# Optimization experiments

Hardware: AMD Instinct MI355X
Metric: run time of the kernel (lower is better)

## Reference

```python
import jax, jax.numpy as jnp
import numpy as np

START_INDEX = 1


def _lstm_cell(x, h, c, W_ih, W_hh, b_ih, b_hh):
    # PyTorch LSTM cell: gate order i, f, g, o
    gates = x @ W_ih.T + b_ih + h @ W_hh.T + b_hh  # [B, 4H]
    i, f, g, o = jnp.split(gates, 4, axis=-1)
    c_new = jax.nn.sigmoid(f) * c + jax.nn.sigmoid(i) * jnp.tanh(g)
    h_new = jax.nn.sigmoid(o) * jnp.tanh(c_new)
    return h_new, c_new


def setup_inputs() -> dict:
    key = jax.random.key(0)
    ks = jax.random.split(key, 13)
    B, C, E, H, V = 32, 512, 512, 512, 32000
    s = 0.05  # keep gates in non-saturated range

    def w(k, shape):
        return jax.random.normal(k, shape, dtype=jnp.float32) * s

    return {
        "context": jax.random.normal(ks[0], (B, C), dtype=jnp.float32),
        "emb": w(ks[1], (V, E)),
        "W_ih_l0": w(ks[2], (4 * H, E + C)),
        "W_hh_l0": w(ks[3], (4 * H, H)),
        "b_ih_l0": w(ks[4], (4 * H,)),
        "b_hh_l0": w(ks[5], (4 * H,)),
        "W_ih_l1": w(ks[6], (4 * H, H)),
        "W_hh_l1": w(ks[7], (4 * H, H)),
        "b_ih_l1": w(ks[8], (4 * H,)),
        "b_hh_l1": w(ks[9], (4 * H,)),
        "W_out": w(ks[10], (V, H)),
        "b_out": w(ks[11], (V,)),
        "max_len": 64,
    }


def reference(context, emb, W_ih_l0, W_hh_l0, b_ih_l0, b_hh_l0,
              W_ih_l1, W_hh_l1, b_ih_l1, b_hh_l1, W_out, b_out, max_len):
    B = context.shape[0]
    H = W_hh_l0.shape[1]
    tok0 = jnp.full((B,), START_INDEX, dtype=jnp.int32)
    z = jnp.zeros((B, H), dtype=context.dtype)

    def step(carry, _):
        tok, h0, c0, h1, c1 = carry
        ex = emb[tok]                                   # [B, E] embedding lookup
        inp = jnp.concatenate([ex, context], axis=-1)   # [B, E+C]
        h0, c0 = _lstm_cell(inp, h0, c0, W_ih_l0, W_hh_l0, b_ih_l0, b_hh_l0)
        h1, c1 = _lstm_cell(h0, h1, c1, W_ih_l1, W_hh_l1, b_ih_l1, b_hh_l1)
        logits = h1 @ W_out.T + b_out                   # [B, V]
        logp = jax.nn.log_softmax(logits, axis=-1)
        tok_next = jnp.argmax(logp, axis=-1).astype(jnp.int32)  # greedy feedback (detached)
        return (tok_next, h0, c0, h1, c1), logp

    _, out = jax.lax.scan(step, (tok0, z, z, z, z), None, length=max_len)
    return jnp.transpose(out, (1, 0, 2))                # [B, max_len, V]
```

## Files before the change

### kernel.cpp

```cpp
#include <hip/hip_runtime.h>
#include <math.h>

#define BB 32
#define HH 512
#define VV 32000
#define TT 64

#define OFF_H0T  0
#define OFF_H1T  32768
#define OFF_C0   65536
#define OFF_C1   81920
#define OFF_PC0  98304
#define OFF_AMAX 163840

__device__ __forceinline__ float sigmoidf_(float x) { return 1.0f / (1.0f + expf(-x)); }

__device__ __forceinline__ float dot4(const float4 wv, const float4 xv) {
    return wv.x * xv.x + wv.y * xv.y + wv.z * xv.z + wv.w * xv.w;
}
__device__ __forceinline__ void bcast_fma(float* A, const float4 wv,
                                          const float4 x0, const float4 x1,
                                          const float4 x2, const float4 x3) {
    A[0] += wv.x * x0.x + wv.y * x1.x + wv.z * x2.x + wv.w * x3.x;
    A[1] += wv.x * x0.y + wv.y * x1.y + wv.z * x2.y + wv.w * x3.y;
    A[2] += wv.x * x0.z + wv.y * x1.z + wv.z * x2.z + wv.w * x3.z;
    A[3] += wv.x * x0.w + wv.y * x1.w + wv.z * x2.w + wv.w * x3.w;
}

__global__ void k_init(float* __restrict__ ws) {
    int idx = blockIdx.x * 256 + threadIdx.x;
    ws[OFF_H0T + idx] = 0.0f;
    ws[OFF_H1T + idx] = 0.0f;
    ws[OFF_C0 + idx]  = 0.0f;
    ws[OFF_C1 + idx]  = 0.0f;
    if (idx < BB) ((unsigned long long*)(ws + OFF_AMAX))[idx] = 0xFFFFFFFEull;
}

__global__ __launch_bounds__(256, 4) void k_pc0(
    const float* __restrict__ Wih0, const float* __restrict__ ctx,
    const float* __restrict__ bih0, const float* __restrict__ bhh0,
    float* __restrict__ pc0)
{
    __shared__ float red[16][16][32];
    const int tid = threadIdx.x;
    const int ks = tid >> 4, bg = (tid >> 2) & 3, rg = tid & 3;
    const int hu = blockIdx.x * 4 + rg;
    const int k0 = ks * 32, b0 = bg * 8;

    float acc[4][8];
#pragma unroll
    for (int g = 0; g < 4; ++g)
#pragma unroll
        for (int j = 0; j < 8; ++j) acc[g][j] = 0.0f;

    const float* wp[4];
#pragma unroll
    for (int g = 0; g < 4; ++g) wp[g] = Wih0 + (size_t)(g * 512 + hu) * 1024 + 512 + k0;

#pragma unroll 2
    for (int kk4 = 0; kk4 < 8; ++kk4) {
        const int kk = kk4 * 4;
        float4 w4[4];
#pragma unroll
        for (int g = 0; g < 4; ++g) w4[g] = *(const float4*)(wp[g] + kk);
#pragma unroll
        for (int j = 0; j < 8; ++j) {
            const float4 xe = *(const float4*)(ctx + (size_t)(b0 + j) * 512 + k0 + kk);
#pragma unroll
            for (int g = 0; g < 4; ++g) acc[g][j] += dot4(w4[g], xe);
        }
    }

#pragma unroll
    for (int g = 0; g < 4; ++g) {
        *(float4*)&red[ks][g * 4 + rg][b0]     = make_float4(acc[g][0], acc[g][1], acc[g][2], acc[g][3]);
        *(float4*)&red[ks][g * 4 + rg][b0 + 4] = make_float4(acc[g][4], acc[g][5], acc[g][6], acc[g][7]);
    }
    __syncthreads();
    if (tid < 128) {
        const int huL = (tid >> 5) & 3, b = tid & 31;
#pragma unroll
        for (int g = 0; g < 4; ++g) {
            float s = 0.0f;
#pragma unroll
            for (int k = 0; k < 16; ++k) s += red[k][g * 4 + huL][b];
            const int row = g * 512 + blockIdx.x * 4 + huL;
            pc0[(size_t)row * 32 + b] = s + bih0[row] + bhh0[row];
        }
    }
}

template <int MODE>
__global__ __launch_bounds__(256, 4) void k_lstm(
    const float* __restrict__ Wa, const float* __restrict__ Wb,
    const float* __restrict__ xA, const float* __restrict__ xB,
    const float* __restrict__ emb,
    const unsigned long long* __restrict__ amax_in,
    const float* __restrict__ pc0,
    const float* __restrict__ bih, const float* __restrict__ bhh,
    float* __restrict__ hT_out, float* __restrict__ c_st,
    unsigned long long* __restrict__ amax_reset)
{
    constexpr int SA = (MODE == 0) ? 1024 : 512;
    __shared__ float red[16][8][32];

    const int tid = threadIdx.x;
    const int ks = tid >> 4, bg = (tid >> 1) & 7, rg = tid & 1;
    const int hu = blockIdx.x * 2 + rg;
    const int b0 = bg * 4;
    const bool partA = (ks < 8);
    const int k0 = (partA ? ks : ks - 8) * 64;

    float acc[4][4];
#pragma unroll
    for (int g = 0; g < 4; ++g)
#pragma unroll
        for (int j = 0; j < 4; ++j) acc[g][j] = 0.0f;

    const float* wp[4];
#pragma unroll
    for (int g = 0; g < 4; ++g)
        wp[g] = partA ? (Wa + (size_t)(g * 512 + hu) * SA + k0)
                      : (Wb + (size_t)(g * 512 + hu) * 512 + k0);

    const float* ep[4];
    if (MODE == 0 && partA) {
#pragma unroll
        for (int j = 0; j < 4; ++j) {
            const int tok = (int)(0xFFFFFFFFu - (unsigned)(amax_in[b0 + j] & 0xFFFFFFFFull));
            ep[j] = emb + (size_t)tok * 512 + k0;
        }
    }
    const float* xb = (partA ? xA : xB) + (size_t)k0 * 32 + b0;

#pragma unroll 2
    for (int kk4 = 0; kk4 < 16; ++kk4) {
        const int kk = kk4 * 4;
        float4 w4[4];
#pragma unroll
        for (int g = 0; g < 4; ++g) w4[g] = *(const float4*)(wp[g] + kk);
        if (MODE == 0 && partA) {
#pragma unroll
            for (int j = 0; j < 4; ++j) {
                const float4 xe = *(const float4*)(ep[j] + kk);
#pragma unroll
                for (int g = 0; g < 4; ++g) acc[g][j] += dot4(w4[g], xe);
            }
        } else {
            const float4 x0 = *(const float4*)(xb + (size_t)(kk + 0) * 32);
            const float4 x1 = *(const float4*)(xb + (size_t)(kk + 1) * 32);
            const float4 x2 = *(const float4*)(xb + (size_t)(kk + 2) * 32);
            const float4 x3 = *(const float4*)(xb + (size_t)(kk + 3) * 32);
#pragma unroll
            for (int g = 0; g < 4; ++g) bcast_fma(acc[g], w4[g], x0, x1, x2, x3);
        }
    }

#pragma unroll
    for (int g = 0; g < 4; ++g)
        *(float4*)&red[ks][g * 2 + rg][b0] = make_float4(acc[g][0], acc[g][1], acc[g][2], acc[g][3]);
    __syncthreads();

    if (tid < 64) {
        const int huL = tid >> 5, b = tid & 31;
        const int hu2 = blockIdx.x * 2 + huL;
        float gate[4];
#pragma unroll
        for (int g = 0; g < 4; ++g) {
            float s = 0.0f;
#pragma unroll
            for (int k = 0; k < 16; ++k) s += red[k][g * 2 + huL][b];
            const int row = g * 512 + hu2;
            if (MODE == 0) s += pc0[(size_t)row * 32 + b];
            else           s += bih[row] + bhh[row];
            gate[g] = s;
        }
        const float gi = sigmoidf_(gate[0]);
        const float gf = sigmoidf_(gate[1]);
        const float gg = tanhf(gate[2]);
        const float go = sigmoidf_(gate[3]);
        const int ci = hu2 * 32 + b;
        const float cn = gf * c_st[ci] + gi * gg;
        c_st[ci] = cn;
        hT_out[ci] = go * tanhf(cn);
    }
    if (MODE == 1) {
        if (tid >= 64 && tid < 96) amax_reset[tid - 64] = 0ull;
    }
}

__global__ __launch_bounds__(256, 4) void k_logits(
    const float* __restrict__ h1T, const float* __restrict__ Wout,
    const float* __restrict__ bout, float* __restrict__ out,
    unsigned long long* __restrict__ amax, int t)
{
    __shared__ float red[8][32][36];
    __shared__ unsigned long long lmax[8][32];

    const int tid = threadIdx.x;
    const int rg = tid & 7, bg = (tid >> 3) & 3, ks = tid >> 5;
    const int row0 = blockIdx.x * 32 + rg * 4;
    const int b0 = bg * 8, k0 = ks * 64;

    float acc[4][8];
#pragma unroll
    for (int i = 0; i < 4; ++i)
#pragma unroll
        for (int j = 0; j < 8; ++j) acc[i][j] = 0.0f;

    const float* wp[4];
#pragma unroll
    for (int i = 0; i < 4; ++i) wp[i] = Wout + (size_t)(row0 + i) * 512 + k0;
    const float* xb = h1T + (size_t)k0 * 32 + b0;

#pragma unroll 2
    for (int kk4 = 0; kk4 < 16; ++kk4) {
        const int kk = kk4 * 4;
        const float4 x00 = *(const float4*)(xb + (size_t)(kk + 0) * 32);
        const float4 x01 = *(const float4*)(xb + (size_t)(kk + 0) * 32 + 4);
        const float4 x10 = *(const float4*)(xb + (size_t)(kk + 1) * 32);
        const float4 x11 = *(const float4*)(xb + (size_t)(kk + 1) * 32 + 4);
        const float4 x20 = *(const float4*)(xb + (size_t)(kk + 2) * 32);
        const float4 x21 = *(const float4*)(xb + (size_t)(kk + 2) * 32 + 4);
        const float4 x30 = *(const float4*)(xb + (size_t)(kk + 3) * 32);
        const float4 x31 = *(const float4*)(xb + (size_t)(kk + 3) * 32 + 4);
#pragma unroll
        for (int i = 0; i < 4; ++i) {
            const float4 w = *(const float4*)(wp[i] + kk);
            bcast_fma(&acc[i][0], w, x00, x10, x20, x30);
            bcast_fma(&acc[i][4], w, x01, x11, x21, x31);
        }
    }

#pragma unroll
    for (int i = 0; i < 4; ++i) {
        *(float4*)&red[ks][rg * 4 + i][b0]     = make_float4(acc[i][0], acc[i][1], acc[i][2], acc[i][3]);
        *(float4*)&red[ks][rg * 4 + i][b0 + 4] = make_float4(acc[i][4], acc[i][5], acc[i][6], acc[i][7]);
    }
    __syncthreads();

    {
        const int r2 = tid & 31, bq = tid >> 5;
        const int row = blockIdx.x * 32 + r2;
        const float bias = bout[row];
#pragma unroll
        for (int j = 0; j < 4; ++j) {
            const int b = bq * 4 + j;
            float v = bias;
#pragma unroll
            for (int k = 0; k < 8; ++k) v += red[k][r2][b];
            out[((size_t)b * TT + t) * VV + row] = v;
        }
    }
    {
        const int b = tid & 31, rq = tid >> 5;
        unsigned long long best = 0ull;
#pragma unroll
        for (int i = 0; i < 4; ++i) {
            const int rr = rq * 4 + i;
            const int row = blockIdx.x * 32 + rr;
            float v = bout[row];
#pragma unroll
            for (int k = 0; k < 8; ++k) v += red[k][rr][b];
            unsigned u = __float_as_uint(v);
            u = (u & 0x80000000u) ? ~u : (u | 0x80000000u);
            const unsigned long long key =
                ((unsigned long long)u << 32) | (unsigned long long)(0xFFFFFFFFu - (unsigned)row);
            best = best > key ? best : key;
        }
        lmax[rq][b] = best;
    }
    __syncthreads();
    if (tid < 32) {
        unsigned long long bb = lmax[0][tid];
#pragma unroll
        for (int q = 1; q < 8; ++q) bb = bb > lmax[q][tid] ? bb : lmax[q][tid];
        if (bb > amax[tid]) atomicMax(&amax[tid], bb);
    }
}

__global__ __launch_bounds__(256) void k_lsm(float* __restrict__ out) {
    float* p = out + (size_t)blockIdx.x * VV;
    const int tid = threadIdx.x;
    __shared__ float sm[4], ss[4];

    float m = -1e30f, s = 0.0f;
    for (int i = tid * 4; i < VV; i += 1024) {
        const float4 v = *(const float4*)(p + i);
        const float cm = fmaxf(fmaxf(v.x, v.y), fmaxf(v.z, v.w));
        const float nm = fmaxf(m, cm);
        s = s * __expf(m - nm) + __expf(v.x - nm) + __expf(v.y - nm)
                               + __expf(v.z - nm) + __expf(v.w - nm);
        m = nm;
    }
#pragma unroll
    for (int off = 32; off > 0; off >>= 1) {
        const float om = __shfl_down(m, off, 64);
        const float os = __shfl_down(s, off, 64);
        const float nm = fmaxf(m, om);
        s = s * __expf(m - nm) + os * __expf(om - nm);
        m = nm;
    }
    if ((tid & 63) == 0) { sm[tid >> 6] = m; ss[tid >> 6] = s; }
    __syncthreads();
    float M = sm[0], S = ss[0];
#pragma unroll
    for (int w = 1; w < 4; ++w) {
        const float nm = fmaxf(M, sm[w]);
        S = S * __expf(M - nm) + ss[w] * __expf(sm[w] - nm);
        M = nm;
    }
    const float lz = M + __logf(S);
    for (int i = tid * 4; i < VV; i += 1024) {
        float4 v = *(const float4*)(p + i);
        v.x -= lz; v.y -= lz; v.z -= lz; v.w -= lz;
        *(float4*)(p + i) = v;
    }
}

extern "C" void kernel_launch(void* const* d_in, const int* in_sizes, int n_in,
                              void* d_out, int out_size, void* d_ws, size_t ws_size,
                              hipStream_t stream) {
    const float* ctx  = (const float*)d_in[0];
    const float* emb  = (const float*)d_in[1];
    const float* Wih0 = (const float*)d_in[2];
    const float* Whh0 = (const float*)d_in[3];
    const float* bih0 = (const float*)d_in[4];
    const float* bhh0 = (const float*)d_in[5];
    const float* Wih1 = (const float*)d_in[6];
    const float* Whh1 = (const float*)d_in[7];
    const float* bih1 = (const float*)d_in[8];
    const float* bhh1 = (const float*)d_in[9];
    const float* Wout = (const float*)d_in[10];
    const float* bout = (const float*)d_in[11];

    float* out = (float*)d_out;
    float* ws  = (float*)d_ws;
    float* h0T[2] = { ws + OFF_H0T, ws + OFF_H0T + 16384 };
    float* h1T[2] = { ws + OFF_H1T, ws + OFF_H1T + 16384 };
    float* c0  = ws + OFF_C0;
    float* c1  = ws + OFF_C1;
    float* pc0 = ws + OFF_PC0;
    unsigned long long* amax = (unsigned long long*)(ws + OFF_AMAX);

    k_init<<<64, 256, 0, stream>>>(ws);
    k_pc0<<<128, 256, 0, stream>>>(Wih0, ctx, bih0, bhh0, pc0);

    for (int t = 0; t < TT; ++t) {
        const int pp = t & 1, nn = pp ^ 1;
        k_lstm<0><<<256, 256, 0, stream>>>(
            Wih0, Whh0, nullptr, h0T[pp], emb, amax, pc0, nullptr, nullptr,
            h0T[nn], c0, nullptr);
        k_lstm<1><<<256, 256, 0, stream>>>(
            Wih1, Whh1, h0T[nn], h1T[pp], emb, nullptr, nullptr, bih1, bhh1,
            h1T[nn], c1, amax);
        k_logits<<<1000, 256, 0, stream>>>(h1T[nn], Wout, bout, out, amax, t);
    }
    k_lsm<<<BB * TT, 256, 0, stream>>>(out);
}
```

Measured before the change: 5.496 ms.

## Fuse per-tile softmax stats into logits kernel and split LSTM across more blocks

The logits kernel now computes a per-tile max and sum-exp for each batch row and writes these pairs to workspace. The final log-softmax kernel then merges 1000 pairs per row instead of re-reading all 32000 logits, which removes one full read pass over the output. The LSTM kernels now use one hidden unit per block over 512 blocks with a finer K split, for more parallelism. Output stores use nontemporal hints and the reduction smem is padded to 35, at the cost of extra workspace and a fallback path when the workspace is too small.

```diff
diff --git a/kernel.cpp b/kernel.cpp
--- a/kernel.cpp
+++ b/kernel.cpp
@@ -5,13 +5,17 @@
 #define HH 512
 #define VV 32000
 #define TT 64
-
-#define OFF_H0T  0
-#define OFF_H1T  32768
-#define OFF_C0   65536
-#define OFF_C1   81920
-#define OFF_PC0  98304
-#define OFF_AMAX 163840
+#define NTILE 1000
+
+#define OFF_H0T   0
+#define OFF_H1T   32768
+#define OFF_C0    65536
+#define OFF_C1    81920
+#define OFF_PC0   98304
+#define OFF_AMAX  163840
+#define OFF_PAIRS 163904
+
+typedef float f32x4_ __attribute__((ext_vector_type(4)));
 
 __device__ __forceinline__ float sigmoidf_(float x) { return 1.0f / (1.0f + expf(-x)); }
 
@@ -102,14 +106,15 @@
     unsigned long long* __restrict__ amax_reset)
 {
     constexpr int SA = (MODE == 0) ? 1024 : 512;
-    __shared__ float red[16][8][32];
+    __shared__ float red[32][4][32];
+    __shared__ float gg[4][32];
 
     const int tid = threadIdx.x;
-    const int ks = tid >> 4, bg = (tid >> 1) & 7, rg = tid & 1;
-    const int hu = blockIdx.x * 2 + rg;
+    const int ks = tid >> 3, bg = tid & 7;
+    const int hu = blockIdx.x;
     const int b0 = bg * 4;
-    const bool partA = (ks < 8);
-    const int k0 = (partA ? ks : ks - 8) * 64;
+    const bool partA = (ks < 16);
+    const int k0 = (partA ? ks : ks - 16) * 32;
 
     float acc[4][4];
 #pragma unroll
@@ -133,8 +138,8 @@
     }
     const float* xb = (partA ? xA : xB) + (size_t)k0 * 32 + b0;
 
-#pragma unroll 2
-    for (int kk4 = 0; kk4 < 16; ++kk4) {
+#pragma unroll 4
+    for (int kk4 = 0; kk4 < 8; ++kk4) {
         const int kk = kk4 * 4;
         float4 w4[4];
 #pragma unroll
@@ -158,29 +163,29 @@
 
 #pragma unroll
     for (int g = 0; g < 4; ++g)
-        *(float4*)&red[ks][g * 2 + rg][b0] = make_float4(acc[g][0], acc[g][1], acc[g][2], acc[g][3]);
-    __syncthreads();
-
-    if (tid < 64) {
-        const int huL = tid >> 5, b = tid & 31;
-        const int hu2 = blockIdx.x * 2 + huL;
-        float gate[4];
-#pragma unroll
-        for (int g = 0; g < 4; ++g) {
-            float s = 0.0f;
-#pragma unroll
-            for (int k = 0; k < 16; ++k) s += red[k][g * 2 + huL][b];
-            const int row = g * 512 + hu2;
-            if (MODE == 0) s += pc0[(size_t)row * 32 + b];
-            else           s += bih[row] + bhh[row];
-            gate[g] = s;
-        }
-        const float gi = sigmoidf_(gate[0]);
-        const float gf = sigmoidf_(gate[1]);
-        const float gg = tanhf(gate[2]);
-        const float go = sigmoidf_(gate[3]);
-        const int ci = hu2 * 32 + b;
-        const float cn = gf * c_st[ci] + gi * gg;
+        *(float4*)&red[ks][g][b0] = make_float4(acc[g][0], acc[g][1], acc[g][2], acc[g][3]);
+    __syncthreads();
+
+    if (tid < 128) {
+        const int g = tid >> 5, b = tid & 31;
+        float s = 0.0f;
+#pragma unroll
+        for (int k = 0; k < 32; ++k) s += red[k][g][b];
+        const int row = g * 512 + hu;
+        if (MODE == 0) s += pc0[(size_t)row * 32 + b];
+        else           s += bih[row] + bhh[row];
+        gg[g][b] = s;
+    }
+    __syncthreads();
+
+    if (tid < 32) {
+        const int b = tid;
+        const float gi = sigmoidf_(gg[0][b]);
+        const float gf = sigmoidf_(gg[1][b]);
+        const float gn = tanhf(gg[2][b]);
+        const float go = sigmoidf_(gg[3][b]);
+        const int ci = hu * 32 + b;
+        const float cn = gf * c_st[ci] + gi * gn;
         c_st[ci] = cn;
         hT_out[ci] = go * tanhf(cn);
     }
@@ -192,10 +197,11 @@
 __global__ __launch_bounds__(256, 4) void k_logits(
     const float* __restrict__ h1T, const float* __restrict__ Wout,
     const float* __restrict__ bout, float* __restrict__ out,
-    unsigned long long* __restrict__ amax, int t)
+    unsigned long long* __restrict__ amax, float* __restrict__ pairs, int t)
 {
-    __shared__ float red[8][32][36];
+    __shared__ float red[8][32][35];
     __shared__ unsigned long long lmax[8][32];
+    __shared__ float pm[8][32], ps[8][32];
 
     const int tid = threadIdx.x;
     const int rg = tid & 7, bg = (tid >> 3) & 3, ks = tid >> 5;
@@ -249,12 +255,13 @@
             float v = bias;
 #pragma unroll
             for (int k = 0; k < 8; ++k) v += red[k][r2][b];
-            out[((size_t)b * TT + t) * VV + row] = v;
+            __builtin_nontemporal_store(v, out + ((size_t)b * TT + t) * VV + row);
         }
     }
     {
         const int b = tid & 31, rq = tid >> 5;
         unsigned long long best = 0ull;
+        float vv[4];
 #pragma unroll
         for (int i = 0; i < 4; ++i) {
             const int rr = rq * 4 + i;
@@ -262,6 +269,7 @@
             float v = bout[row];
 #pragma unroll
             for (int k = 0; k < 8; ++k) v += red[k][rr][b];
+            vv[i] = v;
             unsigned u = __float_as_uint(v);
             u = (u & 0x80000000u) ? ~u : (u | 0x80000000u);
             const unsigned long long key =
@@ -269,6 +277,10 @@
             best = best > key ? best : key;
         }
         lmax[rq][b] = best;
+        const float lm = fmaxf(fmaxf(vv[0], vv[1]), fmaxf(vv[2], vv[3]));
+        ps[rq][b] = __expf(vv[0] - lm) + __expf(vv[1] - lm)
+                  + __expf(vv[2] - lm) + __expf(vv[3] - lm);
+        pm[rq][b] = lm;
     }
     __syncthreads();
     if (tid < 32) {
@@ -276,22 +288,47 @@
 #pragma unroll
         for (int q = 1; q < 8; ++q) bb = bb > lmax[q][tid] ? bb : lmax[q][tid];
         if (bb > amax[tid]) atomicMax(&amax[tid], bb);
-    }
-}
-
-__global__ __launch_bounds__(256) void k_lsm(float* __restrict__ out) {
+        if (pairs) {
+            float M = pm[0][tid], S = ps[0][tid];
+#pragma unroll
+            for (int q = 1; q < 8; ++q) {
+                const float nm = fmaxf(M, pm[q][tid]);
+                S = S * __expf(M - nm) + ps[q][tid] * __expf(pm[q][tid] - nm);
+                M = nm;
+            }
+            float* pr = pairs + ((size_t)t * NTILE + blockIdx.x) * 64;
+            pr[tid] = M;
+            pr[32 + tid] = S;
+        }
+    }
+}
+
+__global__ __launch_bounds__(256) void k_lsm(float* __restrict__ out,
+                                             const float* __restrict__ pairs) {
     float* p = out + (size_t)blockIdx.x * VV;
     const int tid = threadIdx.x;
     __shared__ float sm[4], ss[4];
 
     float m = -1e30f, s = 0.0f;
-    for (int i = tid * 4; i < VV; i += 1024) {
-        const float4 v = *(const float4*)(p + i);
-        const float cm = fmaxf(fmaxf(v.x, v.y), fmaxf(v.z, v.w));
-        const float nm = fmaxf(m, cm);
-        s = s * __expf(m - nm) + __expf(v.x - nm) + __expf(v.y - nm)
-                               + __expf(v.z - nm) + __expf(v.w - nm);
-        m = nm;
+    if (pairs) {
+        const int b = blockIdx.x >> 6, t = blockIdx.x & 63;
+        const float* pr = pairs + (size_t)t * NTILE * 64 + b;
+        for (int tile = tid; tile < NTILE; tile += 256) {
+            const float tm = pr[(size_t)tile * 64];
+            const float ts = pr[(size_t)tile * 64 + 32];
+            const float nm = fmaxf(m, tm);
+            s = s * __expf(m - nm) + ts * __expf(tm - nm);
+            m = nm;
+        }
+    } else {
+        for (int i = tid * 4; i < VV; i += 1024) {
+            const float4 v = *(const float4*)(p + i);
+            const float cm = fmaxf(fmaxf(v.x, v.y), fmaxf(v.z, v.w));
+            const float nm = fmaxf(m, cm);
+            s = s * __expf(m - nm) + __expf(v.x - nm) + __expf(v.y - nm)
+                                   + __expf(v.z - nm) + __expf(v.w - nm);
+            m = nm;
+        }
     }
 #pragma unroll
     for (int off = 32; off > 0; off >>= 1) {
@@ -312,9 +349,9 @@
     }
     const float lz = M + __logf(S);
     for (int i = tid * 4; i < VV; i += 1024) {
-        float4 v = *(const float4*)(p + i);
-        v.x -= lz; v.y -= lz; v.z -= lz; v.w -= lz;
-        *(float4*)(p + i) = v;
+        f32x4_ v = *(const f32x4_*)(p + i);
+        v = v - lz;
+        __builtin_nontemporal_store(v, (f32x4_*)(p + i));
     }
 }
 
@@ -343,18 +380,21 @@
     float* pc0 = ws + OFF_PC0;
     unsigned long long* amax = (unsigned long long*)(ws + OFF_AMAX);
 
+    const size_t need_bytes = (size_t)(OFF_PAIRS + TT * NTILE * 64) * sizeof(float);
+    float* pairs = (ws_size >= need_bytes) ? (ws + OFF_PAIRS) : nullptr;
+
     k_init<<<64, 256, 0, stream>>>(ws);
     k_pc0<<<128, 256, 0, stream>>>(Wih0, ctx, bih0, bhh0, pc0);
 
     for (int t = 0; t < TT; ++t) {
         const int pp = t & 1, nn = pp ^ 1;
-        k_lstm<0><<<256, 256, 0, stream>>>(
+        k_lstm<0><<<512, 256, 0, stream>>>(
             Wih0, Whh0, nullptr, h0T[pp], emb, amax, pc0, nullptr, nullptr,
             h0T[nn], c0, nullptr);
-        k_lstm<1><<<256, 256, 0, stream>>>(
+        k_lstm<1><<<512, 256, 0, stream>>>(
             Wih1, Whh1, h0T[nn], h1T[pp], emb, nullptr, nullptr, bih1, bhh1,
             h1T[nn], c1, amax);
-        k_logits<<<1000, 256, 0, stream>>>(h1T[nn], Wout, bout, out, amax, t);
-    }
-    k_lsm<<<BB * TT, 256, 0, stream>>>(out);
-}
+        k_logits<<<1000, 256, 0, stream>>>(h1T[nn], Wout, bout, out, amax, pairs, t);
+    }
+    k_lsm<<<BB * TT, 256, 0, stream>>>(out, pairs);
+}
```

Measured after the change: 5.898 ms. +7.3%, slower.
